# Kernel optimization log

Measured on AMD Instinct MI355X. Metric: run time of the kernel, lower is better.

## Reference

```python
import jax, jax.numpy as jnp
import numpy as np

B, V_IN, V_OUT, F_IN, F_OUT, N_CP = 100000, 128, 128, 512, 512, 16
DIM_H = max(V_IN, V_OUT)  # hidden_vectors=None -> max(dim_vectors_in, dim_vectors_out)
EPS = 1e-8


def setup_inputs() -> dict:
    key = jax.random.key(0)
    ks = jax.random.split(key, 9)
    u = lambda k, shape, scale: jax.random.uniform(k, shape, jnp.float32, -scale, scale)
    wh_k = 1.0 / np.sqrt(V_IN).astype(np.float32)
    wu_k = 1.0 / np.sqrt(DIM_H + N_CP).astype(np.float32)
    f_in = DIM_H + N_CP + F_IN  # 656
    kf = 1.0 / np.sqrt(f_in).astype(np.float32)
    kg = 1.0 / np.sqrt(F_OUT).astype(np.float32)
    return {
        "feats": jax.random.normal(ks[0], (B, F_IN), jnp.float32),
        "vectors": jax.random.normal(ks[1], (B, V_IN, 3), jnp.float32),
        "Wh": u(ks[2], (V_IN, DIM_H), wh_k),
        "Wcp": u(ks[3], (V_IN, 2 * N_CP), wh_k),
        "Wu": u(ks[4], (DIM_H + N_CP, V_OUT), wu_k),
        "Wf": u(ks[5], (f_in, F_OUT), kf),      # torch Linear weight, stored (in,out)
        "bf": u(ks[6], (F_OUT,), kf),
        "Wg": u(ks[7], (F_OUT, V_OUT), kg),
        "bg": u(ks[8], (V_OUT,), kg),
    }


def reference(feats, vectors, Wh, Wcp, Wu, Wf, bf, Wg, bg):
    # vectors: [b, v_in, 3]; mix vector channels (matmul acts per xyz component c)
    Vh = jnp.einsum('bvc,vh->bhc', vectors, Wh)            # [b, dim_h, 3]
    # cross-product features
    Vcp = jnp.einsum('bvc,vp->bpc', vectors, Wcp)          # [b, 2*n_cp, 3]
    cp = jnp.cross(Vcp[:, :N_CP], Vcp[:, N_CP:])           # [b, n_cp, 3]
    Vh = jnp.concatenate([Vh, cp], axis=1)                 # [b, dim_h+n_cp, 3]
    Vu = jnp.einsum('bkc,ko->boc', Vh, Wu)                 # [b, v_out, 3]
    # clamped L2 norm over xyz
    sh = jnp.sqrt(jnp.maximum(jnp.sum(Vh * Vh, axis=-1), EPS))  # [b, dim_h+n_cp]
    s = jnp.concatenate([feats, sh], axis=1)               # [b, dim_h+n_cp+f_in]
    feats_out = jax.nn.silu(s @ Wf + bf)                   # [b, f_out]
    gating = feats_out @ Wg + bg                           # [b, v_out]
    vectors_out = jax.nn.sigmoid(gating)[..., None] * Vu   # [b, v_out, 3]
    return feats_out, vectors_out
```

## Files before the change

### kernel.cpp

```cpp
#include <hip/hip_runtime.h>

#define BATCH 100000
#define M3 300000
#define VECBASE 51200000
#define KP 704

typedef float fl4  __attribute__((ext_vector_type(4)));
typedef float f32x4 __attribute__((ext_vector_type(4)));
typedef short s16x4 __attribute__((ext_vector_type(4)));
typedef short s16x8 __attribute__((ext_vector_type(8)));

__device__ __forceinline__ short f2bf(float f) {
  unsigned int u = __float_as_uint(f);
  u += 0x7fffu + ((u >> 16) & 1u);
  return (short)(u >> 16);
}
__device__ __forceinline__ float bf2f(short s) {
  return __uint_as_float(((unsigned int)(unsigned short)s) << 16);
}
__device__ __forceinline__ s16x8 pack8(fl4 a, fl4 b) {
  s16x8 o;
  o[0] = f2bf(a[0]); o[1] = f2bf(a[1]); o[2] = f2bf(a[2]); o[3] = f2bf(a[3]);
  o[4] = f2bf(b[0]); o[5] = f2bf(b[1]); o[6] = f2bf(b[2]); o[7] = f2bf(b[3]);
  return o;
}
__device__ __forceinline__ void glds16(const void* g, void* l) {
  __builtin_amdgcn_global_load_lds((const __attribute__((address_space(1))) void*)g,
                                   (__attribute__((address_space(3))) void*)l, 16, 0, 0);
}
#define WAITBAR(N) asm volatile("s_waitcnt vmcnt(" #N ")\ns_barrier" ::: "memory")
#define RAWBAR()   asm volatile("s_barrier" ::: "memory")

__global__ __launch_bounds__(256) void prep_w(
    const float* __restrict__ feats, const float* __restrict__ Wh,
    const float* __restrict__ Wcp, const float* __restrict__ Wu,
    const float* __restrict__ Wf, const float* __restrict__ Wg,
    short* __restrict__ Ab, short* __restrict__ WB1, short* __restrict__ WuTp,
    short* __restrict__ WfT, short* __restrict__ WgT) {
  const int tid = blockIdx.x * 256 + threadIdx.x;
  const int stride = gridDim.x * 256;
  for (int i = tid; i < 6400000; i += stride) {
    int b = i >> 6, kk = (i & 63) * 8;
    fl4 v0 = *reinterpret_cast<const fl4*>(&feats[(size_t)b * 512 + kk]);
    fl4 v1 = *reinterpret_cast<const fl4*>(&feats[(size_t)b * 512 + kk + 4]);
    *(s16x8*)&Ab[(size_t)b * KP + kk] = pack8(v0, v1);
  }
  for (int gid = tid; gid < 466944; gid += stride) {
    if (gid < 20480) {
      int n = gid >> 7, k = gid & 127;
      WB1[gid] = f2bf(n < 128 ? Wh[k * 128 + n] : Wcp[k * 32 + (n - 128)]);
    } else if (gid < 40960) {
      int i = gid - 20480;
      int o = i / 160, k = i - o * 160;
      WuTp[i] = k < 144 ? f2bf(Wu[k * 128 + o]) : (short)0;
    } else if (gid < 401408) {
      int i = gid - 40960;
      int n = i / KP, k = i - n * KP;
      WfT[i] = k < 656 ? f2bf(Wf[k * 512 + n]) : (short)0;
    } else {
      int i = gid - 401408;
      int n = i >> 9, k = i & 511;
      WgT[i] = f2bf(Wg[k * 128 + n]);
    }
  }
}

__global__ __launch_bounds__(256) void geo_fused(
    const float* __restrict__ vecs, const short* __restrict__ WB1,
    const short* __restrict__ WuTp, short* __restrict__ Ab,
    short* __restrict__ Vub) {
  __shared__ __align__(16) short U[192 * 168];
  const int t = threadIdx.x;
  const int b0 = blockIdx.x * 64;
  const int row0 = blockIdx.x * 192;

#pragma unroll
  for (int it = 0; it < 8; ++it) {
    int fi = (it * 256 + t) * 12;
    int bl = fi / 384;
    int rem = fi - bl * 384;
    int v0 = rem / 3;
    int b = b0 + bl;
    fl4 x = (fl4){0.f, 0.f, 0.f, 0.f}, y = x, z = x;
    if (b < BATCH) {
      const float* p = &vecs[(size_t)b * 384 + rem];
      x = *(const fl4*)p; y = *(const fl4*)(p + 4); z = *(const fl4*)(p + 8);
    }
    float vc[3][4] = {{x[0], x[3], y[2], z[1]},
                      {x[1], y[0], y[3], z[2]},
                      {x[2], y[1], z[0], z[3]}};
#pragma unroll
    for (int c = 0; c < 3; ++c) {
      int row = bl * 3 + c;
      s16x4 q;
#pragma unroll
      for (int e = 0; e < 4; ++e) q[e] = f2bf(vc[c][e]);
      int off = (row << 8) + (v0 << 1);
      *(s16x4*)((char*)U + (off ^ ((row & 7) << 4))) = q;
    }
  }
  __syncthreads();

  const int lane = t & 63, wv = t >> 6;
  const int wr = wv >> 1, wc = wv & 1;
  const int lr = lane & 15, lk = lane >> 4;

  {
    f32x4 acc[6][5];
#pragma unroll
    for (int i = 0; i < 6; ++i)
#pragma unroll
      for (int j = 0; j < 5; ++j) acc[i][j] = (f32x4){0.f, 0.f, 0.f, 0.f};
#pragma unroll
    for (int kk = 0; kk < 4; ++kk) {
      s16x8 af[6], bq[5];
#pragma unroll
      for (int mi = 0; mi < 6; ++mi) {
        int row = wr * 96 + mi * 16 + lr;
        int off = (row << 8) + (kk << 6) + (lk << 4);
        af[mi] = *(const s16x8*)((const char*)U + (off ^ ((row & 7) << 4)));
      }
#pragma unroll
      for (int ni = 0; ni < 5; ++ni)
        bq[ni] = *reinterpret_cast<const s16x8*>(
            &WB1[(wc * 80 + ni * 16 + lr) * 128 + (kk << 5) + (lk << 3)]);
      __builtin_amdgcn_s_setprio(1);
#pragma unroll
      for (int mi = 0; mi < 6; ++mi)
#pragma unroll
        for (int ni = 0; ni < 5; ++ni)
          acc[mi][ni] = __builtin_amdgcn_mfma_f32_16x16x32_bf16(af[mi], bq[ni], acc[mi][ni], 0, 0, 0);
      __builtin_amdgcn_s_setprio(0);
    }
    __syncthreads();
#pragma unroll
    for (int mi = 0; mi < 6; ++mi)
#pragma unroll
      for (int ni = 0; ni < 5; ++ni) {
        int col = wc * 80 + ni * 16 + lr;
#pragma unroll
        for (int r = 0; r < 4; ++r) {
          int row = wr * 96 + mi * 16 + lk * 4 + r;
          U[row * 168 + col] = f2bf(acc[mi][ni][r]);
        }
      }
  }
  __syncthreads();

  {
    int bl = t >> 2, pj = t & 3;
    int gb = b0 + bl;
    float shcp[4];
#pragma unroll
    for (int q = 0; q < 4; ++q) {
      int p = pj * 4 + q;
      float ax = bf2f(U[(bl * 3 + 0) * 168 + 128 + p]);
      float ay = bf2f(U[(bl * 3 + 1) * 168 + 128 + p]);
      float az = bf2f(U[(bl * 3 + 2) * 168 + 128 + p]);
      float bx = bf2f(U[(bl * 3 + 0) * 168 + 144 + p]);
      float by = bf2f(U[(bl * 3 + 1) * 168 + 144 + p]);
      float bz = bf2f(U[(bl * 3 + 2) * 168 + 144 + p]);
      float cx = ay * bz - az * by;
      float cy = az * bx - ax * bz;
      float cz = ax * by - ay * bx;
      U[(bl * 3 + 0) * 168 + 128 + p] = f2bf(cx);
      U[(bl * 3 + 1) * 168 + 128 + p] = f2bf(cy);
      U[(bl * 3 + 2) * 168 + 128 + p] = f2bf(cz);
      U[(bl * 3 + 0) * 168 + 144 + p] = 0;
      U[(bl * 3 + 1) * 168 + 144 + p] = 0;
      U[(bl * 3 + 2) * 168 + 144 + p] = 0;
      shcp[q] = sqrtf(fmaxf(cx * cx + cy * cy + cz * cz, 1e-8f));
    }
    if (gb < BATCH) {
#pragma unroll
      for (int q = 0; q < 4; ++q)
        Ab[(size_t)gb * KP + 512 + 128 + pj * 4 + q] = f2bf(shcp[q]);
#pragma unroll
      for (int z = 0; z < 12; ++z)
        Ab[(size_t)gb * KP + 512 + 144 + pj * 12 + z] = 0;
    }
  }
  {
    int bl = t >> 2, kq = t & 3;
    int gb = b0 + bl;
    if (gb < BATCH) {
#pragma unroll
      for (int j = 0; j < 4; ++j) {
        int k = kq * 32 + j * 8;
        s16x8 r0 = *(const s16x8*)&U[(bl * 3 + 0) * 168 + k];
        s16x8 r1 = *(const s16x8*)&U[(bl * 3 + 1) * 168 + k];
        s16x8 r2 = *(const s16x8*)&U[(bl * 3 + 2) * 168 + k];
        s16x8 o;
#pragma unroll
        for (int e = 0; e < 8; ++e) {
          float x = bf2f(r0[e]), y = bf2f(r1[e]), z = bf2f(r2[e]);
          o[e] = f2bf(sqrtf(fmaxf(x * x + y * y + z * z, 1e-8f)));
        }
        *(s16x8*)&Ab[(size_t)gb * KP + 512 + k] = o;
      }
    }
  }
  __syncthreads();

  {
    f32x4 acc2[6][4];
#pragma unroll
    for (int i = 0; i < 6; ++i)
#pragma unroll
      for (int j = 0; j < 4; ++j) acc2[i][j] = (f32x4){0.f, 0.f, 0.f, 0.f};
#pragma unroll
    for (int kk = 0; kk < 5; ++kk) {
      s16x8 af[6], bq[4];
#pragma unroll
      for (int mi = 0; mi < 6; ++mi) {
        int row = wr * 96 + mi * 16 + lr;
        af[mi] = *(const s16x8*)&U[row * 168 + (kk << 5) + (lk << 3)];
      }
#pragma unroll
      for (int ni = 0; ni < 4; ++ni)
        bq[ni] = *reinterpret_cast<const s16x8*>(
            &WuTp[(wc * 64 + ni * 16 + lr) * 160 + (kk << 5) + (lk << 3)]);
      __builtin_amdgcn_s_setprio(1);
#pragma unroll
      for (int mi = 0; mi < 6; ++mi)
#pragma unroll
        for (int ni = 0; ni < 4; ++ni)
          acc2[mi][ni] = __builtin_amdgcn_mfma_f32_16x16x32_bf16(af[mi], bq[ni], acc2[mi][ni], 0, 0, 0);
      __builtin_amdgcn_s_setprio(0);
    }
#pragma unroll
    for (int mi = 0; mi < 6; ++mi)
#pragma unroll
      for (int ni = 0; ni < 4; ++ni) {
        int col = wc * 64 + ni * 16 + lr;
#pragma unroll
        for (int r = 0; r < 4; ++r) {
          int row = row0 + wr * 96 + mi * 16 + lk * 4 + r;
          if (row < M3) Vub[(size_t)row * 128 + col] = f2bf(acc2[mi][ni][r]);
        }
      }
  }
}

__global__ __launch_bounds__(512, 4) void gemm_feats(
    const short* __restrict__ Ab, const short* __restrict__ WfT,
    const float* __restrict__ bfv, float* __restrict__ out,
    short* __restrict__ fob) {
  const int bid = blockIdx.x;
  const int xcd = bid & 7, bi = bid >> 3;
  const int swz = (xcd < 4 ? xcd * 196 : 784 + (xcd - 4) * 195) + bi;
  const int mt = swz >> 1, nt = swz & 1;
  const int row0 = mt << 7, n0 = nt << 8;
  const int t = threadIdx.x;
  const int lane = t & 63, wv = t >> 6;
  const int wr = wv >> 2, wc = wv & 3;
  const int lr = lane & 15, lk = lane >> 4;

  __shared__ __align__(16) short S[(128 + 256) * 32];
  short* As = S;
  short* Bs = S + 4096;

  const int arow = t >> 2, ach = t & 3;
  const short* srcA = &Ab[(size_t)min(row0 + arow, BATCH - 1) * KP + (ach ^ ((arow >> 1) & 3)) * 8];
  const int adof = t * 8;
  const short* srcB[2];
  int bdof[2];
#pragma unroll
  for (int j = 0; j < 2; ++j) {
    int cid = j * 512 + t;
    int brow = cid >> 2, bch = cid & 3;
    srcB[j] = &WfT[(size_t)(n0 + brow) * KP + (bch ^ ((brow >> 1) & 3)) * 8];
    bdof[j] = cid * 8;
  }

  f32x4 acc[4][4];
#pragma unroll
  for (int i = 0; i < 4; ++i)
#pragma unroll
    for (int j = 0; j < 4; ++j) acc[i][j] = (f32x4){0.f, 0.f, 0.f, 0.f};

  for (int ks = 0; ks < 22; ++ks) {
    const int k0 = ks << 5;
    __syncthreads();
    glds16(srcA + k0, &As[adof]);
    glds16(srcB[0] + k0, &Bs[bdof[0]]);
    glds16(srcB[1] + k0, &Bs[bdof[1]]);
    __syncthreads();
    s16x8 af[4], bq[4];
#pragma unroll
    for (int mi = 0; mi < 4; ++mi) {
      int rw = wr * 64 + mi * 16 + lr;
      af[mi] = *(const s16x8*)&As[rw * 32 + (lk ^ ((rw >> 1) & 3)) * 8];
    }
#pragma unroll
    for (int ni = 0; ni < 4; ++ni) {
      int rn = wc * 64 + ni * 16 + lr;
      bq[ni] = *(const s16x8*)&Bs[rn * 32 + (lk ^ ((rn >> 1) & 3)) * 8];
    }
    __builtin_amdgcn_s_setprio(1);
#pragma unroll
    for (int mi = 0; mi < 4; ++mi)
#pragma unroll
      for (int ni = 0; ni < 4; ++ni)
        acc[mi][ni] = __builtin_amdgcn_mfma_f32_16x16x32_bf16(af[mi], bq[ni], acc[mi][ni], 0, 0, 0);
    __builtin_amdgcn_s_setprio(0);
  }

  float* Ls = (float*)S;
#pragma unroll
  for (int g = 0; g < 8; ++g) {
    __syncthreads();
    if (wr == (g >> 2)) {
      int mi = g & 3;
#pragma unroll
      for (int ni = 0; ni < 4; ++ni) {
        int colL = wc * 64 + ni * 16 + lr;
        float bb = bfv[n0 + colL];
#pragma unroll
        for (int rr = 0; rr < 4; ++rr) {
          float x = acc[mi][ni][rr] + bb;
          Ls[(lk * 4 + rr) * 256 + colL] = x / (1.f + __expf(-x));
        }
      }
    }
    __syncthreads();
    {
      int rowL = t >> 5, seg = t & 31;
      int grow = row0 + g * 16 + rowL;
      if (grow < BATCH) {
        const float* p = &Ls[rowL * 256 + seg * 8];
        fl4 a = *(const fl4*)p, b = *(const fl4*)(p + 4);
        float* po = &out[(size_t)grow * 512 + n0 + seg * 8];
        *(fl4*)po = a; *(fl4*)(po + 4) = b;
        *(s16x8*)&fob[(size_t)grow * 512 + n0 + seg * 8] = pack8(a, b);
      }
    }
  }
}

__global__ __launch_bounds__(256) void gemm_gate(
    const short* __restrict__ fob, const short* __restrict__ WgT,
    const float* __restrict__ bg, const short* __restrict__ Vub,
    float* __restrict__ out) {
  const int bid = blockIdx.x;
  const int xcd = bid & 7, bidx = bid >> 3;
  const int swz = (xcd < 6 ? xcd * 98 : 6 * 98 + (xcd - 6) * 97) + bidx;
  const int row0 = swz << 7;
  const int t = threadIdx.x;
  const int lane = t & 63, wv = t >> 6;
  const int wr = wv >> 1, wc = wv & 1;
  const int lr = lane & 15, lk = lane >> 4;

  __shared__ __align__(16) short As[3][128 * 32];
  __shared__ __align__(16) short Bs[3][128 * 32];

  const short* srcA[2];
  const short* srcB[2];
  int dofs[2];
#pragma unroll
  for (int j = 0; j < 2; ++j) {
    int cid = j * 256 + t;
    int row = cid >> 2, ch = cid & 3;
    int chs = ch ^ ((row >> 1) & 3);
    srcA[j] = &fob[(size_t)min(row0 + row, BATCH - 1) * 512 + chs * 8];
    srcB[j] = &WgT[(size_t)row * 512 + chs * 8];
    dofs[j] = cid * 8;
  }

  f32x4 acc[4][4];
#pragma unroll
  for (int i = 0; i < 4; ++i)
#pragma unroll
    for (int j = 0; j < 4; ++j) acc[i][j] = (f32x4){0.f, 0.f, 0.f, 0.f};

  auto STAGE = [&](int buf, int ks) {
    const int k0 = ks << 5;
#pragma unroll
    for (int j = 0; j < 2; ++j) glds16(srcA[j] + k0, &As[buf][dofs[j]]);
#pragma unroll
    for (int j = 0; j < 2; ++j) glds16(srcB[j] + k0, &Bs[buf][dofs[j]]);
  };
  auto COMPUTE = [&](int buf) {
    s16x8 af[4], bq[4];
#pragma unroll
    for (int mi = 0; mi < 4; ++mi) {
      int rw = wr * 64 + mi * 16 + lr;
      af[mi] = *(const s16x8*)&As[buf][rw * 32 + (lk ^ ((rw >> 1) & 3)) * 8];
    }
#pragma unroll
    for (int ni = 0; ni < 4; ++ni) {
      int rw = wc * 64 + ni * 16 + lr;
      bq[ni] = *(const s16x8*)&Bs[buf][rw * 32 + (lk ^ ((rw >> 1) & 3)) * 8];
    }
    __builtin_amdgcn_s_setprio(1);
#pragma unroll
    for (int mi = 0; mi < 4; ++mi)
#pragma unroll
      for (int ni = 0; ni < 4; ++ni)
        acc[mi][ni] = __builtin_amdgcn_mfma_f32_16x16x32_bf16(af[mi], bq[ni], acc[mi][ni], 0, 0, 0);
    __builtin_amdgcn_s_setprio(0);
  };

  STAGE(0, 0);
  STAGE(1, 1);
  for (int ks = 0; ks < 16; ++ks) {
    if (ks + 2 < 16) STAGE((ks + 2) % 3, ks + 2);
    if (ks < 14)      WAITBAR(8);
    else if (ks == 14) WAITBAR(4);
    else               WAITBAR(0);
    COMPUTE(ks % 3);
    RAWBAR();
  }

#pragma unroll
  for (int ni = 0; ni < 4; ++ni) {
    int col = wc * 64 + ni * 16 + lr;
    float bb = bg[col];
#pragma unroll
    for (int mi = 0; mi < 4; ++mi) {
      int rbase = row0 + wr * 64 + mi * 16 + lk * 4;
#pragma unroll
      for (int rr = 0; rr < 4; ++rr) {
        int gr = rbase + rr;
        if (gr < BATCH) {
          float x = acc[mi][ni][rr] + bb;
          float gate = 1.f / (1.f + __expf(-x));
          size_t vb = (size_t)(3 * gr) * 128 + col;
          float* po = &out[VECBASE + ((size_t)gr * 128 + col) * 3];
          po[0] = gate * bf2f(Vub[vb]);
          po[1] = gate * bf2f(Vub[vb + 128]);
          po[2] = gate * bf2f(Vub[vb + 256]);
        }
      }
    }
  }
}

extern "C" void kernel_launch(void* const* d_in, const int* in_sizes, int n_in,
                              void* d_out, int out_size, void* d_ws, size_t ws_size,
                              hipStream_t stream) {
  const float* feats = (const float*)d_in[0];
  const float* vecs  = (const float*)d_in[1];
  const float* Wh    = (const float*)d_in[2];
  const float* Wcp   = (const float*)d_in[3];
  const float* Wu    = (const float*)d_in[4];
  const float* Wf    = (const float*)d_in[5];
  const float* bfv   = (const float*)d_in[6];
  const float* Wg    = (const float*)d_in[7];
  const float* bg    = (const float*)d_in[8];
  float* out = (float*)d_out;

  char* ws = (char*)d_ws;
  short* Ab   = (short*)ws;
  short* Vub  = (short*)(ws + 140800000);
  short* fob  = (short*)(ws + 217600000);
  short* WfT  = (short*)(ws + 320000000);
  short* WgT  = (short*)(ws + 320720896);
  short* WB1  = (short*)(ws + 320851968);
  short* WuTp = (short*)(ws + 320892928);

  hipLaunchKernelGGL(prep_w,     dim3(2048), dim3(256), 0, stream,
                     feats, Wh, Wcp, Wu, Wf, Wg, Ab, WB1, WuTp, WfT, WgT);
  hipLaunchKernelGGL(geo_fused,  dim3(1563), dim3(256), 0, stream,
                     vecs, WB1, WuTp, Ab, Vub);
  hipLaunchKernelGGL(gemm_feats, dim3(1564), dim3(512), 0, stream,
                     Ab, WfT, bfv, out, fob);
  hipLaunchKernelGGL(gemm_gate,  dim3(782),  dim3(256), 0, stream,
                     fob, WgT, bg, Vub, out);
}
```

Before: 458.5 us.

## Double K-step depth in both GEMMs and enlarge gate tiles to 256 rows

gemm_feats now stages 64-wide K slices with an 8-way XOR swizzle, which halves the number of barrier-bracketed iterations. gemm_gate drops its triple-buffered async pipeline for a simpler single-buffer loop with 64-wide K steps, 256-row tiles, 512 threads and half the blocks. The aim is to amortize sync and load overhead across more MFMA work per barrier. In exchange it uses more LDS per block and loses the load/compute overlap the gate kernel previously had.

Result: faster. 432.9 us (-5.6%).

```diff
diff --git a/kernel.cpp b/kernel.cpp
--- a/kernel.cpp
+++ b/kernel.cpp
@@ -28,8 +28,6 @@
   __builtin_amdgcn_global_load_lds((const __attribute__((address_space(1))) void*)g,
                                    (__attribute__((address_space(3))) void*)l, 16, 0, 0);
 }
-#define WAITBAR(N) asm volatile("s_waitcnt vmcnt(" #N ")\ns_barrier" ::: "memory")
-#define RAWBAR()   asm volatile("s_barrier" ::: "memory")
 
 __global__ __launch_bounds__(256) void prep_w(
     const float* __restrict__ feats, const float* __restrict__ Wh,
@@ -256,20 +254,24 @@
   const int wr = wv >> 2, wc = wv & 3;
   const int lr = lane & 15, lk = lane >> 4;
 
-  __shared__ __align__(16) short S[(128 + 256) * 32];
+  __shared__ __align__(16) short S[(128 + 256) * 64];
   short* As = S;
-  short* Bs = S + 4096;
-
-  const int arow = t >> 2, ach = t & 3;
-  const short* srcA = &Ab[(size_t)min(row0 + arow, BATCH - 1) * KP + (ach ^ ((arow >> 1) & 3)) * 8];
-  const int adof = t * 8;
-  const short* srcB[2];
-  int bdof[2];
+  short* Bs = S + 128 * 64;
+
+  const short* srcA[2]; int adof[2];
 #pragma unroll
   for (int j = 0; j < 2; ++j) {
     int cid = j * 512 + t;
-    int brow = cid >> 2, bch = cid & 3;
-    srcB[j] = &WfT[(size_t)(n0 + brow) * KP + (bch ^ ((brow >> 1) & 3)) * 8];
+    int row = cid >> 3, ch = cid & 7;
+    srcA[j] = &Ab[(size_t)min(row0 + row, BATCH - 1) * KP + (ch ^ (row & 7)) * 8];
+    adof[j] = cid * 8;
+  }
+  const short* srcB[4]; int bdof[4];
+#pragma unroll
+  for (int j = 0; j < 4; ++j) {
+    int cid = j * 512 + t;
+    int row = cid >> 3, ch = cid & 7;
+    srcB[j] = &WfT[(size_t)(n0 + row) * KP + (ch ^ (row & 7)) * 8];
     bdof[j] = cid * 8;
   }
 
@@ -279,31 +281,35 @@
 #pragma unroll
     for (int j = 0; j < 4; ++j) acc[i][j] = (f32x4){0.f, 0.f, 0.f, 0.f};
 
-  for (int ks = 0; ks < 22; ++ks) {
-    const int k0 = ks << 5;
-    __syncthreads();
-    glds16(srcA + k0, &As[adof]);
-    glds16(srcB[0] + k0, &Bs[bdof[0]]);
-    glds16(srcB[1] + k0, &Bs[bdof[1]]);
-    __syncthreads();
-    s16x8 af[4], bq[4];
-#pragma unroll
-    for (int mi = 0; mi < 4; ++mi) {
-      int rw = wr * 64 + mi * 16 + lr;
-      af[mi] = *(const s16x8*)&As[rw * 32 + (lk ^ ((rw >> 1) & 3)) * 8];
-    }
-#pragma unroll
-    for (int ni = 0; ni < 4; ++ni) {
-      int rn = wc * 64 + ni * 16 + lr;
-      bq[ni] = *(const s16x8*)&Bs[rn * 32 + (lk ^ ((rn >> 1) & 3)) * 8];
-    }
-    __builtin_amdgcn_s_setprio(1);
-#pragma unroll
-    for (int mi = 0; mi < 4; ++mi)
-#pragma unroll
-      for (int ni = 0; ni < 4; ++ni)
-        acc[mi][ni] = __builtin_amdgcn_mfma_f32_16x16x32_bf16(af[mi], bq[ni], acc[mi][ni], 0, 0, 0);
-    __builtin_amdgcn_s_setprio(0);
+  for (int ks = 0; ks < 11; ++ks) {
+    const int k0 = ks << 6;
+    __syncthreads();
+    glds16(srcA[0] + k0, &As[adof[0]]);
+    glds16(srcA[1] + k0, &As[adof[1]]);
+#pragma unroll
+    for (int j = 0; j < 4; ++j) glds16(srcB[j] + k0, &Bs[bdof[j]]);
+    __syncthreads();
+#pragma unroll
+    for (int kk = 0; kk < 2; ++kk) {
+      s16x8 af[4], bq[4];
+#pragma unroll
+      for (int mi = 0; mi < 4; ++mi) {
+        int rw = wr * 64 + mi * 16 + lr;
+        af[mi] = *(const s16x8*)&As[rw * 64 + (((kk << 2) + lk) ^ (rw & 7)) * 8];
+      }
+#pragma unroll
+      for (int ni = 0; ni < 4; ++ni) {
+        int rn = wc * 64 + ni * 16 + lr;
+        bq[ni] = *(const s16x8*)&Bs[rn * 64 + (((kk << 2) + lk) ^ (rn & 7)) * 8];
+      }
+      __builtin_amdgcn_s_setprio(1);
+#pragma unroll
+      for (int mi = 0; mi < 4; ++mi)
+#pragma unroll
+        for (int ni = 0; ni < 4; ++ni)
+          acc[mi][ni] = __builtin_amdgcn_mfma_f32_16x16x32_bf16(af[mi], bq[ni], acc[mi][ni], 0, 0, 0);
+      __builtin_amdgcn_s_setprio(0);
+    }
   }
 
   float* Ls = (float*)S;
@@ -338,33 +344,38 @@
   }
 }
 
-__global__ __launch_bounds__(256) void gemm_gate(
+__global__ __launch_bounds__(512, 4) void gemm_gate(
     const short* __restrict__ fob, const short* __restrict__ WgT,
     const float* __restrict__ bg, const short* __restrict__ Vub,
     float* __restrict__ out) {
   const int bid = blockIdx.x;
-  const int xcd = bid & 7, bidx = bid >> 3;
-  const int swz = (xcd < 6 ? xcd * 98 : 6 * 98 + (xcd - 6) * 97) + bidx;
-  const int row0 = swz << 7;
+  const int xcd = bid & 7, bi = bid >> 3;
+  const int swz = (xcd < 7 ? xcd * 49 : 343 + (xcd - 7) * 48) + bi;
+  const int row0 = swz << 8;
   const int t = threadIdx.x;
   const int lane = t & 63, wv = t >> 6;
   const int wr = wv >> 1, wc = wv & 1;
   const int lr = lane & 15, lk = lane >> 4;
 
-  __shared__ __align__(16) short As[3][128 * 32];
-  __shared__ __align__(16) short Bs[3][128 * 32];
-
-  const short* srcA[2];
-  const short* srcB[2];
-  int dofs[2];
+  __shared__ __align__(16) short S[(256 + 128) * 64];
+  short* As = S;
+  short* Bs = S + 256 * 64;
+
+  const short* srcA[4]; int adof[4];
+#pragma unroll
+  for (int j = 0; j < 4; ++j) {
+    int cid = j * 512 + t;
+    int row = cid >> 3, ch = cid & 7;
+    srcA[j] = &fob[(size_t)min(row0 + row, BATCH - 1) * 512 + (ch ^ (row & 7)) * 8];
+    adof[j] = cid * 8;
+  }
+  const short* srcB[2]; int bdof[2];
 #pragma unroll
   for (int j = 0; j < 2; ++j) {
-    int cid = j * 256 + t;
-    int row = cid >> 2, ch = cid & 3;
-    int chs = ch ^ ((row >> 1) & 3);
-    srcA[j] = &fob[(size_t)min(row0 + row, BATCH - 1) * 512 + chs * 8];
-    srcB[j] = &WgT[(size_t)row * 512 + chs * 8];
-    dofs[j] = cid * 8;
+    int cid = j * 512 + t;
+    int row = cid >> 3, ch = cid & 7;
+    srcB[j] = &WgT[(size_t)row * 512 + (ch ^ (row & 7)) * 8];
+    bdof[j] = cid * 8;
   }
 
   f32x4 acc[4][4];
@@ -373,43 +384,35 @@
 #pragma unroll
     for (int j = 0; j < 4; ++j) acc[i][j] = (f32x4){0.f, 0.f, 0.f, 0.f};
 
-  auto STAGE = [&](int buf, int ks) {
-    const int k0 = ks << 5;
-#pragma unroll
-    for (int j = 0; j < 2; ++j) glds16(srcA[j] + k0, &As[buf][dofs[j]]);
-#pragma unroll
-    for (int j = 0; j < 2; ++j) glds16(srcB[j] + k0, &Bs[buf][dofs[j]]);
-  };
-  auto COMPUTE = [&](int buf) {
-    s16x8 af[4], bq[4];
-#pragma unroll
-    for (int mi = 0; mi < 4; ++mi) {
-      int rw = wr * 64 + mi * 16 + lr;
-      af[mi] = *(const s16x8*)&As[buf][rw * 32 + (lk ^ ((rw >> 1) & 3)) * 8];
-    }
-#pragma unroll
-    for (int ni = 0; ni < 4; ++ni) {
-      int rw = wc * 64 + ni * 16 + lr;
-      bq[ni] = *(const s16x8*)&Bs[buf][rw * 32 + (lk ^ ((rw >> 1) & 3)) * 8];
-    }
-    __builtin_amdgcn_s_setprio(1);
-#pragma unroll
-    for (int mi = 0; mi < 4; ++mi)
-#pragma unroll
-      for (int ni = 0; ni < 4; ++ni)
-        acc[mi][ni] = __builtin_amdgcn_mfma_f32_16x16x32_bf16(af[mi], bq[ni], acc[mi][ni], 0, 0, 0);
-    __builtin_amdgcn_s_setprio(0);
-  };
-
-  STAGE(0, 0);
-  STAGE(1, 1);
-  for (int ks = 0; ks < 16; ++ks) {
-    if (ks + 2 < 16) STAGE((ks + 2) % 3, ks + 2);
-    if (ks < 14)      WAITBAR(8);
-    else if (ks == 14) WAITBAR(4);
-    else               WAITBAR(0);
-    COMPUTE(ks % 3);
-    RAWBAR();
+  for (int ks = 0; ks < 8; ++ks) {
+    const int k0 = ks << 6;
+    __syncthreads();
+#pragma unroll
+    for (int j = 0; j < 4; ++j) glds16(srcA[j] + k0, &As[adof[j]]);
+    glds16(srcB[0] + k0, &Bs[bdof[0]]);
+    glds16(srcB[1] + k0, &Bs[bdof[1]]);
+    __syncthreads();
+#pragma unroll
+    for (int kk = 0; kk < 2; ++kk) {
+      s16x8 af[4], bq[4];
+#pragma unroll
+      for (int mi = 0; mi < 4; ++mi) {
+        int rw = wr * 64 + mi * 16 + lr;
+        af[mi] = *(const s16x8*)&As[rw * 64 + (((kk << 2) + lk) ^ (rw & 7)) * 8];
+      }
+#pragma unroll
+      for (int ni = 0; ni < 4; ++ni) {
+        int rn = wc * 64 + ni * 16 + lr;
+        bq[ni] = *(const s16x8*)&Bs[rn * 64 + (((kk << 2) + lk) ^ (rn & 7)) * 8];
+      }
+      __builtin_amdgcn_s_setprio(1);
+#pragma unroll
+      for (int mi = 0; mi < 4; ++mi)
+#pragma unroll
+        for (int ni = 0; ni < 4; ++ni)
+          acc[mi][ni] = __builtin_amdgcn_mfma_f32_16x16x32_bf16(af[mi], bq[ni], acc[mi][ni], 0, 0, 0);
+      __builtin_amdgcn_s_setprio(0);
+    }
   }
 
 #pragma unroll
@@ -465,6 +468,6 @@
                      vecs, WB1, WuTp, Ab, Vub);
   hipLaunchKernelGGL(gemm_feats, dim3(1564), dim3(512), 0, stream,
                      Ab, WfT, bfv, out, fob);
-  hipLaunchKernelGGL(gemm_gate,  dim3(782),  dim3(256), 0, stream,
+  hipLaunchKernelGGL(gemm_gate,  dim3(391),  dim3(512), 0, stream,
                      fob, WgT, bg, Vub, out);
 }
```
